# Kernel optimization log

Hardware: AMD Instinct MI355X
Metric: run time of the kernel (lower is better)

The kernel has to match this reference:

```python
import jax, jax.numpy as jnp
import numpy as np

B = 64      # num graphs
NPG = 800   # nodes per graph
N = B * NPG
EPG = 6400  # edges per graph (avg degree 8)
APG = 64    # feasible actions per graph
H = 4       # attention heads
C = 64      # hidden channels per head
OUT = 128   # out_channels


def _gat_params(key, fin, h, c, concat):
    k1, k2, k3 = jax.random.split(key, 3)
    s = 1.0 / np.sqrt(fin)
    W = jax.random.uniform(k1, (fin, h * c), jnp.float32, -s, s)
    a_src = jax.random.uniform(k2, (h, c), jnp.float32, -s, s)
    a_dst = jax.random.uniform(k3, (h, c), jnp.float32, -s, s)
    b = jnp.zeros((h * c if concat else c,), jnp.float32)
    return W, a_src, a_dst, b


def _lin_params(key, fin, fout):
    k1, k2 = jax.random.split(key)
    s = 1.0 / np.sqrt(fin)
    W = jax.random.uniform(k1, (fin, fout), jnp.float32, -s, s)
    b = jax.random.uniform(k2, (fout,), jnp.float32, -s, s)
    return W, b


def setup_inputs() -> dict:
    key = jax.random.key(0)
    ks = list(jax.random.split(key, 24))
    x = jax.random.normal(ks[0], (N, 5), jnp.float32)
    offs = jnp.arange(B, dtype=jnp.int32) * NPG
    src = jax.random.randint(ks[1], (B, EPG), 0, NPG, jnp.int32) + offs[:, None]
    dst = jax.random.randint(ks[2], (B, EPG), 0, NPG, jnp.int32) + offs[:, None]
    edge_index = jnp.stack([src.reshape(-1), dst.reshape(-1)])
    batch = jnp.repeat(jnp.arange(B, dtype=jnp.int32), NPG)
    actions_idx = (jax.random.randint(ks[3], (B, APG, 2), 0, NPG, jnp.int32)
                   + offs[:, None, None]).reshape(-1, 2)
    tabu_label = (jax.random.uniform(ks[4], (B * APG, 1)) < 0.5).astype(jnp.float32)
    inp = dict(x=x, edge_index=edge_index, batch=batch,
               actions_idx=actions_idx, tabu_label=tabu_label)
    names = ['f1', 'f2', 'f3', 'b1', 'b2', 'b3']
    fins = [3, H * C, H * C, 3, H * C, H * C]
    hs = [H, H, 1, H, H, 1]
    cs = [C, C, OUT, C, C, OUT]
    concats = [True, True, False, True, True, False]
    for i, nm in enumerate(names):
        W, a_s, a_d, b = _gat_params(ks[5 + i], fins[i], hs[i], cs[i], concats[i])
        inp[nm + '_W'] = W; inp[nm + '_as'] = a_s; inp[nm + '_ad'] = a_d; inp[nm + '_b'] = b
    dims = [(8 * OUT + 1, 2 * OUT), (2 * OUT, 2 * OUT), (2 * OUT, 2 * OUT), (2 * OUT, 1)]
    for i, (fi, fo) in enumerate(dims):
        W, b = _lin_params(ks[12 + i], fi, fo)
        inp['p_W%d' % (i + 1)] = W; inp['p_b%d' % (i + 1)] = b
    return inp


def _gat(h, s, d, W, a_src, a_dst, bias, concat):
    # PyG GATConv: project, per-edge attention, softmax over target index, scatter-add
    n = h.shape[0]
    Hh, Cc = a_src.shape
    xp = (h @ W).reshape(n, Hh, Cc)                      # [N,H,C]
    al_s = (xp * a_src).sum(-1)                          # [N,H]
    al_d = (xp * a_dst).sum(-1)                          # [N,H]
    e = jax.nn.leaky_relu(al_s[s] + al_d[d], 0.2)        # [E,H]
    m = jax.ops.segment_max(e, d, num_segments=n)
    ex = jnp.exp(e - m[d])
    den = jax.ops.segment_sum(ex, d, num_segments=n)
    alpha = ex / (den[d] + 1e-16)
    out = jax.ops.segment_sum(xp[s] * alpha[..., None], d, num_segments=n)  # [N,H,C]
    out = out.reshape(n, Hh * Cc) if concat else out.mean(axis=1)
    return out + bias


def reference(x, edge_index, batch, actions_idx, tabu_label,
              f1_W, f1_as, f1_ad, f1_b, f2_W, f2_as, f2_ad, f2_b,
              f3_W, f3_as, f3_ad, f3_b, b1_W, b1_as, b1_ad, b1_b,
              b2_W, b2_as, b2_ad, b2_b, b3_W, b3_as, b3_ad, b3_b,
              p_W1, p_b1, p_W2, p_b2, p_W3, p_b3, p_W4, p_b4):
    n = x.shape[0]
    ar = jnp.arange(n, dtype=edge_index.dtype)
    ei = jnp.concatenate([edge_index, jnp.stack([ar, ar])], axis=1)  # add_self_loops
    src, dst = ei[0], ei[1]
    # forward branch (flow source_to_target)
    hf = x[:, jnp.array([0, 1, 3])]
    hf = jax.nn.elu(_gat(hf, src, dst, f1_W, f1_as, f1_ad, f1_b, True))
    hf = jax.nn.elu(_gat(hf, src, dst, f2_W, f2_as, f2_ad, f2_b, True))
    hf3 = _gat(hf, src, dst, f3_W, f3_as, f3_ad, f3_b, False)
    # backward branch (flow target_to_source == reversed edges)
    hb = x[:, jnp.array([0, 2, 4])]
    hb = jax.nn.elu(_gat(hb, dst, src, b1_W, b1_as, b1_ad, b1_b, True))
    hb = jax.nn.elu(_gat(hb, dst, src, b2_W, b2_as, b2_ad, b2_b, True))
    hb3 = _gat(hb, dst, src, b3_W, b3_as, b3_ad, b3_b, False)
    h_node = jnp.concatenate([hf3, hb3], axis=-1)        # [N, 2*OUT]
    counts = jax.ops.segment_sum(jnp.ones((n,), x.dtype), batch, num_segments=B)
    g_pool = jax.ops.segment_sum(h_node, batch, num_segments=B) / counts[:, None]
    node_h = jnp.concatenate([h_node, g_pool[batch]], axis=-1)  # [N, 4*OUT]
    action_h = jnp.concatenate([node_h[actions_idx[:, 0]],
                                node_h[actions_idx[:, 1]],
                                tabu_label], axis=-1)    # [A, 8*OUT+1]
    h = jnp.tanh(action_h @ p_W1 + p_b1)
    h = jnp.tanh(h @ p_W2 + p_b2)
    h = jnp.tanh(h @ p_W3 + p_b3)
    score = (h @ p_W4 + p_b4).reshape(B, APG)
    log_prob = jax.nn.log_softmax(score, axis=-1)        # [B, APG]
    entropy = -(jnp.exp(log_prob) * log_prob).sum(-1, keepdims=True)  # [B,1]
    return (log_prob, entropy)
```

## Files before the change

kernel.cpp:

```cpp
#include <hip/hip_runtime.h>
#include <hip/hip_bf16.h>
#include <math.h>

constexpr int NN  = 51200;
constexpr int EE  = 409600;
constexpr int BB  = 64;
constexpr int APG = 64;
constexpr int NPG = 800;
constexpr int SCAN_N = 2 * NN;
constexpr int NA = BB * APG;
constexpr int KF = 1056;

typedef __bf16 bf16x8 __attribute__((ext_vector_type(8)));
typedef float f32x4 __attribute__((ext_vector_type(4)));
typedef float f32x2 __attribute__((ext_vector_type(2)));
typedef __attribute__((address_space(1))) const void g_void;
typedef __attribute__((address_space(3))) void l_void;

__device__ __forceinline__ float leaky(float x) { return x > 0.f ? x : 0.2f * x; }
__device__ __forceinline__ float bflo(unsigned w) { return __uint_as_float(w << 16); }
__device__ __forceinline__ float bfhi(unsigned w) { return __uint_as_float(w & 0xffff0000u); }
__device__ __forceinline__ unsigned short f2b(float x) {
  __hip_bfloat16 h = __float2bfloat16(x);
  unsigned short u;
  __builtin_memcpy(&u, &h, 2);
  return u;
}

__global__ void count_kernel(const int* __restrict__ ei, int* cnt) {
  int e = blockIdx.x * blockDim.x + threadIdx.x;
  if (e >= EE) return;
  int s = ei[e], d = ei[EE + e];
  atomicAdd(&cnt[d], 1);
  atomicAdd(&cnt[NN + s], 1);
}

__global__ __launch_bounds__(256) void scan1_kernel(const int* __restrict__ cnt,
                                                    int* __restrict__ rp,
                                                    int* __restrict__ bsum) {
  __shared__ int wsum[4];
  int b = blockIdx.x, t = threadIdx.x;
  int base = b * 1024 + t * 4;
  int4 v = *(const int4*)(cnt + base);
  int s = v.x + v.y + v.z + v.w;
  int lane = t & 63, wv = t >> 6;
  int incl = s;
  for (int off = 1; off < 64; off <<= 1) {
    int u = __shfl_up(incl, off);
    if (lane >= off) incl += u;
  }
  if (lane == 63) wsum[wv] = incl;
  __syncthreads();
  int woff = 0;
  for (int i = 0; i < wv; i++) woff += wsum[i];
  int excl = woff + incl - s;
  rp[base] = excl;
  rp[base + 1] = excl + v.x;
  rp[base + 2] = excl + v.x + v.y;
  rp[base + 3] = excl + v.x + v.y + v.z;
  if (t == 255) bsum[b] = woff + incl;
}

__global__ void scan2_kernel(const int* __restrict__ bsum, int* __restrict__ boff,
                             int* __restrict__ rp) {
  __shared__ int w0;
  int t = threadIdx.x;
  int v = (t < 100) ? bsum[t] : 0;
  int lane = t & 63;
  int incl = v;
  for (int off = 1; off < 64; off <<= 1) {
    int u = __shfl_up(incl, off);
    if (lane >= off) incl += u;
  }
  if (t == 63) w0 = incl;
  __syncthreads();
  int excl = incl - v + ((t >= 64) ? w0 : 0);
  if (t < 100) boff[t] = excl;
  if (t == 99) rp[SCAN_N] = excl + v;
}

__global__ __launch_bounds__(256) void scan3_kernel(int* __restrict__ rp,
                                                    const int* __restrict__ boff) {
  int b = blockIdx.x;
  int off = boff[b];
  int i = b * 1024 + threadIdx.x * 4;
  int4 v = *(int4*)(rp + i);
  v.x += off; v.y += off; v.z += off; v.w += off;
  *(int4*)(rp + i) = v;
}

__global__ void fill_kernel(const int* __restrict__ ei, const int* __restrict__ rp,
                            int* pos, int* __restrict__ col) {
  int e = blockIdx.x * blockDim.x + threadIdx.x;
  if (e >= EE) return;
  int s = ei[e], d = ei[EE + e];
  int p = atomicAdd(&pos[d], 1);
  col[rp[d] + p] = s;
  int q = atomicAdd(&pos[NN + s], 1);
  col[rp[NN + s] + q] = d;
}

__global__ __launch_bounds__(256) void lin1_al_kernel(const float* __restrict__ x,
                                                      const float* __restrict__ Wf,
                                                      const float* __restrict__ Wb,
                                                      const float* __restrict__ asf,
                                                      const float* __restrict__ asb,
                                                      const float* __restrict__ adf,
                                                      const float* __restrict__ adb,
                                                      __hip_bfloat16* __restrict__ out,
                                                      float* __restrict__ al_s,
                                                      float* __restrict__ al_d) {
  int n = blockIdx.x;
  bool bwd = n >= NN;
  int node = bwd ? n - NN : n;
  const float* W = bwd ? Wb : Wf;
  const float* a_src = bwd ? asb : asf;
  const float* a_dst = bwd ? adb : adf;
  int c1 = bwd ? 2 : 1, c2 = bwd ? 4 : 3;
  int j = threadIdx.x;
  int wv = j >> 6, lane = j & 63;
  float f0 = x[node * 5], f1 = x[node * 5 + c1], f2 = x[node * 5 + c2];
  float v = f0 * W[j] + f1 * W[256 + j] + f2 * W[512 + j];
  out[(size_t)n * 256 + j] = __float2bfloat16(v);
  float ps = v * a_src[j], pd = v * a_dst[j];
  for (int off = 1; off < 64; off <<= 1) {
    ps += __shfl_xor(ps, off);
    pd += __shfl_xor(pd, off);
  }
  if (lane == 0) {
    al_s[n * 4 + wv] = ps;
    al_d[n * 4 + wv] = pd;
  }
}

template <int HH>
__global__ __launch_bounds__(256) void alpha_kernel(const float* __restrict__ als,
                                                    const float* __restrict__ ald,
                                                    const int* __restrict__ rp,
                                                    const int* __restrict__ col,
                                                    float* __restrict__ alpha,
                                                    float* __restrict__ alpha_self) {
  int b = blockIdx.x;
  int xcd = b & 7, q = b >> 3;
  int g2 = (q / 25) * 8 + xcd;
  int d = g2 * 800 + (q % 25) * 32 + (threadIdx.x >> 3);
  int slot = threadIdx.x & 7;
  int off_row = (d >= NN) ? NN : 0;
  float ald_loc[HH], self_lg[HH];
#pragma unroll
  for (int h = 0; h < HH; h++) {
    ald_loc[h] = ald[d * HH + h];
    self_lg[h] = leaky(als[d * HH + h] + ald_loc[h]);
  }
  int beg = rp[d], end = rp[d + 1];
  int i0 = beg + slot;
  bool have = i0 < end;
  int s0 = col[have ? i0 : beg] + off_row;
  float mx[HH], lg0[HH];
#pragma unroll
  for (int h = 0; h < HH; h++) mx[h] = self_lg[h];
  if (have) {
#pragma unroll
    for (int h = 0; h < HH; h++) {
      lg0[h] = leaky(als[s0 * HH + h] + ald_loc[h]);
      mx[h] = fmaxf(mx[h], lg0[h]);
    }
  }
  for (int i = i0 + 8; i < end; i += 8) {
    int s = col[i] + off_row;
#pragma unroll
    for (int h = 0; h < HH; h++) mx[h] = fmaxf(mx[h], leaky(als[s * HH + h] + ald_loc[h]));
  }
#pragma unroll
  for (int h = 0; h < HH; h++) {
    mx[h] = fmaxf(mx[h], __shfl_xor(mx[h], 1));
    mx[h] = fmaxf(mx[h], __shfl_xor(mx[h], 2));
    mx[h] = fmaxf(mx[h], __shfl_xor(mx[h], 4));
  }
  float sm[HH], w0[HH];
#pragma unroll
  for (int h = 0; h < HH; h++) sm[h] = 0.f;
  if (have) {
#pragma unroll
    for (int h = 0; h < HH; h++) {
      w0[h] = __expf(lg0[h] - mx[h]);
      sm[h] += w0[h];
    }
  }
  for (int i = i0 + 8; i < end; i += 8) {
    int s = col[i] + off_row;
#pragma unroll
    for (int h = 0; h < HH; h++) {
      float w = __expf(leaky(als[s * HH + h] + ald_loc[h]) - mx[h]);
      sm[h] += w;
      alpha[(size_t)i * HH + h] = w;
    }
  }
#pragma unroll
  for (int h = 0; h < HH; h++) {
    sm[h] += __shfl_xor(sm[h], 1);
    sm[h] += __shfl_xor(sm[h], 2);
    sm[h] += __shfl_xor(sm[h], 4);
  }
  float inv[HH];
#pragma unroll
  for (int h = 0; h < HH; h++)
    inv[h] = 1.f / (sm[h] + __expf(self_lg[h] - mx[h]) + 1e-16f);
  if (have) {
#pragma unroll
    for (int h = 0; h < HH; h++) alpha[(size_t)i0 * HH + h] = w0[h] * inv[h];
  }
  for (int i = i0 + 8; i < end; i += 8)
#pragma unroll
    for (int h = 0; h < HH; h++) alpha[(size_t)i * HH + h] *= inv[h];
  if (slot == 0) {
#pragma unroll
    for (int h = 0; h < HH; h++)
      alpha_self[d * HH + h] = __expf(self_lg[h] - mx[h]) * inv[h];
  }
}

template <int ND>
__device__ __forceinline__ void load_dw(const unsigned* p, unsigned* w) {
  if constexpr (ND == 4) {
    uint4 v = *(const uint4*)p;
    w[0] = v.x; w[1] = v.y; w[2] = v.z; w[3] = v.w;
  } else {
    uint2 v = *(const uint2*)p;
    w[0] = v.x; w[1] = v.y;
  }
}
__device__ __forceinline__ f32x2 unpk(unsigned w) {
  f32x2 v;
  v.x = bflo(w);
  v.y = bfhi(w);
  return v;
}

template <int HH, int CC, int OUT_SPLIT>
__global__ __launch_bounds__(256) void spmm_kernel(const __hip_bfloat16* __restrict__ xp,
                                                   const float* __restrict__ alpha,
                                                   const float* __restrict__ alpha_self,
                                                   const int* __restrict__ rp,
                                                   const int* __restrict__ col,
                                                   const float* __restrict__ biasf,
                                                   const float* __restrict__ biasb,
                                                   __hip_bfloat16* __restrict__ out_bf,
                                                   int do_elu) {
  constexpr int HC = HH * CC;
  constexpr int CPL = HC / 32;
  constexpr int NW = CPL / 2;
  int b = blockIdx.x;
  int xcd = b & 7, q = b >> 3;
  int g2 = (q / 200) * 8 + xcd;
  int d = g2 * 800 + (q % 200) * 4 + (threadIdx.x >> 6);
  int off_row = (d >= NN) ? NN : 0;
  const float* bias = (d >= NN) ? biasb : biasf;
  int lane = threadIdx.x & 63;
  int sub = lane & 31, g = lane >> 5;
  int h_l = (sub * CPL) / CC;
  const unsigned* xw = (const unsigned*)xp;
  size_t rowoff = (size_t)sub * NW;
  f32x2 acc[NW];
#pragma unroll
  for (int j = 0; j < NW; j++) acc[j] = (f32x2)(0.f);
  int beg = rp[d], end = rp[d + 1];
  int deg = end - beg;
  if (g == 0) {
    float a = alpha_self[d * HH + h_l];
    unsigned w[NW];
    load_dw<NW>(xw + (size_t)d * (HC / 2) + rowoff, w);
#pragma unroll
    for (int q2 = 0; q2 < NW; q2++) acc[q2] += a * unpk(w[q2]);
  }
  for (int it = 0; it * 4 < deg; it++) {
    int e1 = beg + it * 4 + g;
    int e2 = e1 + 2;
    bool p1 = e1 < end, p2 = e2 < end;
    int ec1 = p1 ? e1 : beg, ec2 = p2 ? e2 : beg;
    int s1 = col[ec1] + off_row, s2 = col[ec2] + off_row;
    float a1 = p1 ? alpha[(size_t)ec1 * HH + h_l] : 0.f;
    float a2 = p2 ? alpha[(size_t)ec2 * HH + h_l] : 0.f;
    unsigned w1[NW], w2[NW];
    load_dw<NW>(xw + (size_t)s1 * (HC / 2) + rowoff, w1);
    load_dw<NW>(xw + (size_t)s2 * (HC / 2) + rowoff, w2);
#pragma unroll
    for (int q2 = 0; q2 < NW; q2++)
      acc[q2] += a1 * unpk(w1[q2]) + a2 * unpk(w2[q2]);
  }
#pragma unroll
  for (int j = 0; j < NW; j++) {
    acc[j].x += __shfl_xor(acc[j].x, 32);
    acc[j].y += __shfl_xor(acc[j].y, 32);
  }
  if (g == 0) {
    float v[CPL];
#pragma unroll
    for (int j = 0; j < NW; j++) {
      v[2 * j] = acc[j].x + bias[sub * CPL + 2 * j];
      v[2 * j + 1] = acc[j].y + bias[sub * CPL + 2 * j + 1];
    }
    if (do_elu) {
#pragma unroll
      for (int j = 0; j < CPL; j++) v[j] = v[j] > 0.f ? v[j] : (__expf(v[j]) - 1.f);
    }
    unsigned* ob;
    if constexpr (OUT_SPLIT) {
      int nd = (d < NN) ? d : d - NN;
      int oo = (d < NN) ? 0 : 64;
      ob = (unsigned*)out_bf + (size_t)nd * 128 + oo + sub * NW;
    } else {
      ob = (unsigned*)out_bf + (size_t)d * (HC / 2) + rowoff;
    }
#pragma unroll
    for (int q2 = 0; q2 < NW; q2++)
      ob[q2] = (unsigned)f2b(v[2 * q2]) | ((unsigned)f2b(v[2 * q2 + 1]) << 16);
  }
}

__global__ void castW2_kernel(const float* __restrict__ W0, const float* __restrict__ W1,
                              __hip_bfloat16* __restrict__ Wt0,
                              __hip_bfloat16* __restrict__ Wt1,
                              int K, int N, int Kp) {
  int idx = blockIdx.x * 256 + threadIdx.x;
  int tot = N * Kp;
  if (idx >= 2 * tot) return;
  const float* W = (idx < tot) ? W0 : W1;
  __hip_bfloat16* Wt = (idx < tot) ? Wt0 : Wt1;
  int i = (idx < tot) ? idx : idx - tot;
  int n = i / Kp, k = i % Kp;
  Wt[i] = (k < K) ? __float2bfloat16(W[(size_t)k * N + n]) : __float2bfloat16(0.f);
}

template <int EPI, int ALH, int ALCC>
__global__ __launch_bounds__(256) void gemm_mfma(const __hip_bfloat16* __restrict__ A,
                                                 const __hip_bfloat16* __restrict__ Bt0,
                                                 const __hip_bfloat16* __restrict__ Bt1,
                                                 __hip_bfloat16* __restrict__ Cb,
                                                 const float* __restrict__ bias0,
                                                 const float* __restrict__ bias1,
                                                 const float* __restrict__ asv0,
                                                 const float* __restrict__ asv1,
                                                 const float* __restrict__ adv0,
                                                 const float* __restrict__ adv1,
                                                 float* __restrict__ al_s,
                                                 float* __restrict__ al_d,
                                                 int M, int N, int K, int Mhalf) {
  __shared__ __align__(16) __hip_bfloat16 As[128 * 32];
  __shared__ __align__(16) __hip_bfloat16 Bs[128 * 32];
  int t = threadIdx.x;
  int wave = t >> 6, lane = t & 63;
  int wm = (wave >> 1) * 64, wn = (wave & 1) * 64;
  int bm = blockIdx.y * 128, bn = blockIdx.x * 128;
  bool second = bm >= Mhalf;
  const __hip_bfloat16* Bt = second ? Bt1 : Bt0;
  const float* bias = second ? bias1 : bias0;
  const float* asv = second ? asv1 : asv0;
  const float* adv = second ? adv1 : adv0;

  int r0 = t >> 2, c0 = (t & 3) * 8;
  const __hip_bfloat16* Ag0 = A + (size_t)(bm + r0) * K + c0;
  const __hip_bfloat16* Ag1 = A + (size_t)(bm + r0 + 64) * K + c0;
  const __hip_bfloat16* Bg0 = Bt + (size_t)(bn + r0) * K + c0;
  const __hip_bfloat16* Bg1 = Bt + (size_t)(bn + r0 + 64) * K + c0;
  __hip_bfloat16* Asp0 = As + t * 8;
  __hip_bfloat16* Asp1 = As + 64 * 8 * 4 + t * 8;
  __hip_bfloat16* Bsp0 = Bs + t * 8;
  __hip_bfloat16* Bsp1 = Bs + 64 * 8 * 4 + t * 8;

  f32x4 acc[4][4];
#pragma unroll
  for (int i = 0; i < 4; i++)
#pragma unroll
    for (int j = 0; j < 4; j++) acc[i][j] = (f32x4)(0.f);

  int frag_off = (lane & 15) * 32 + (lane >> 4) * 8;
  const __hip_bfloat16* Ab = As + wm * 32 + frag_off;
  const __hip_bfloat16* Bb = Bs + wn * 32 + frag_off;

  for (int k0 = 0; k0 < K; k0 += 32) {
    __syncthreads();
    __builtin_amdgcn_global_load_lds((g_void*)(Ag0 + k0), (l_void*)Asp0, 16, 0, 0);
    __builtin_amdgcn_global_load_lds((g_void*)(Ag1 + k0), (l_void*)Asp1, 16, 0, 0);
    __builtin_amdgcn_global_load_lds((g_void*)(Bg0 + k0), (l_void*)Bsp0, 16, 0, 0);
    __builtin_amdgcn_global_load_lds((g_void*)(Bg1 + k0), (l_void*)Bsp1, 16, 0, 0);
    __syncthreads();
    bf16x8 af[4], bfr[4];
#pragma unroll
    for (int i = 0; i < 4; i++) af[i] = *(const bf16x8*)(Ab + i * 16 * 32);
#pragma unroll
    for (int j = 0; j < 4; j++) bfr[j] = *(const bf16x8*)(Bb + j * 16 * 32);
#pragma unroll
    for (int i = 0; i < 4; i++)
#pragma unroll
      for (int j = 0; j < 4; j++)
        acc[i][j] = __builtin_amdgcn_mfma_f32_16x16x32_bf16(af[i], bfr[j], acc[i][j], 0, 0, 0);
  }

  int cr = (lane >> 4) * 4, cc = lane & 15;

  if constexpr (ALH > 0) {
    int head = (bn + wn) / ALCC;
    float as_c[4], ad_c[4];
#pragma unroll
    for (int j = 0; j < 4; j++) {
      int colx = bn + wn + j * 16 + cc;
      as_c[j] = asv[colx];
      ad_c[j] = adv[colx];
    }
#pragma unroll
    for (int i = 0; i < 4; i++)
#pragma unroll
      for (int r = 0; r < 4; r++) {
        float ps = 0.f, pd = 0.f;
#pragma unroll
        for (int j = 0; j < 4; j++) {
          ps += acc[i][j][r] * as_c[j];
          pd += acc[i][j][r] * ad_c[j];
        }
        ps += __shfl_xor(ps, 1); pd += __shfl_xor(pd, 1);
        ps += __shfl_xor(ps, 2); pd += __shfl_xor(pd, 2);
        ps += __shfl_xor(ps, 4); pd += __shfl_xor(pd, 4);
        ps += __shfl_xor(ps, 8); pd += __shfl_xor(pd, 8);
        if ((lane & 15) == 0) {
          int row = bm + wm + i * 16 + cr + r;
          if (ALCC > 64) {
            atomicAdd(&al_s[row * ALH + head], ps);
            atomicAdd(&al_d[row * ALH + head], pd);
          } else {
            al_s[row * ALH + head] = ps;
            al_d[row * ALH + head] = pd;
          }
        }
      }
  }

#pragma unroll
  for (int i = 0; i < 4; i++)
#pragma unroll
    for (int j = 0; j < 4; j++) {
      int colx = bn + wn + j * 16 + cc;
      float bs = (EPI == 2) ? bias[colx] : 0.f;
#pragma unroll
      for (int r = 0; r < 4; r++) {
        float v = acc[i][j][r];
        if (EPI == 2) v = tanhf(v + bs);
        Cb[(size_t)(bm + wm + i * 16 + cr + r) * N + colx] = __float2bfloat16(v);
      }
    }
}

__global__ void pool1_kernel(const __hip_bfloat16* __restrict__ h_node,
                             float* __restrict__ part) {
  int g = blockIdx.y, c = blockIdx.x, t = threadIdx.x;
  const unsigned* base = (const unsigned*)h_node + ((size_t)g * NPG + c * 100) * 128 + t;
  f32x2 s = (f32x2)(0.f);
  for (int i = 0; i < 100; i++) {
    unsigned w = base[(size_t)i * 128];
    s += unpk(w);
  }
  part[(size_t)(g * 8 + c) * 256 + 2 * t] = s.x;
  part[(size_t)(g * 8 + c) * 256 + 2 * t + 1] = s.y;
}

__global__ void pool2_kernel(const float* __restrict__ part, float* __restrict__ g_pool) {
  int g = blockIdx.x, t = threadIdx.x;
  float s = 0.f;
  for (int c = 0; c < 8; c++) s += part[(size_t)(g * 8 + c) * 256 + t];
  g_pool[g * 256 + t] = s * (1.f / NPG);
}

__global__ __launch_bounds__(256) void buildfeat_kernel(const __hip_bfloat16* __restrict__ h_node,
                                                        const float* __restrict__ g_pool,
                                                        const int* __restrict__ actions,
                                                        const float* __restrict__ tabu,
                                                        const int* __restrict__ batch,
                                                        __hip_bfloat16* __restrict__ feat) {
  int a = (blockIdx.x * blockDim.x + threadIdx.x) >> 6;
  int lane = threadIdx.x & 63;
  if (a >= NA) return;
  int n0 = actions[a * 2], n1 = actions[a * 2 + 1];
  int g = batch[n0];
  ushort4 v0 = *(const ushort4*)(h_node + (size_t)n0 * 256 + lane * 4);
  float4 vg = *(const float4*)(g_pool + (size_t)g * 256 + lane * 4);
  ushort4 v1 = *(const ushort4*)(h_node + (size_t)n1 * 256 + lane * 4);
  __hip_bfloat16* fr = feat + (size_t)a * KF;
  ushort4 ug = make_ushort4(f2b(vg.x), f2b(vg.y), f2b(vg.z), f2b(vg.w));
  *(ushort4*)(fr + lane * 4) = v0;
  *(ushort4*)(fr + 256 + lane * 4) = ug;
  *(ushort4*)(fr + 512 + lane * 4) = v1;
  *(ushort4*)(fr + 768 + lane * 4) = ug;
  if (lane < 8) {
    float t0 = (lane == 0) ? tabu[a] : 0.f;
    ushort4 u = make_ushort4(f2b(t0), 0, 0, 0);
    *(ushort4*)(fr + 1024 + lane * 4) = u;
  }
}

__global__ __launch_bounds__(256) void gemv_kernel(const __hip_bfloat16* __restrict__ y,
                                                   const float* __restrict__ W4,
                                                   const float* __restrict__ b4,
                                                   float* __restrict__ scores) {
  int a = (blockIdx.x * blockDim.x + threadIdx.x) >> 6;
  int lane = threadIdx.x & 63;
  if (a >= NA) return;
  const unsigned* row = (const unsigned*)(y + (size_t)a * 256);
  float s = 0.f;
#pragma unroll
  for (int q = 0; q < 2; q++) {
    unsigned w = row[lane * 2 + q];
    s += bflo(w) * W4[lane * 4 + 2 * q] + bfhi(w) * W4[lane * 4 + 2 * q + 1];
  }
  for (int off = 1; off < 64; off <<= 1) s += __shfl_xor(s, off);
  if (lane == 0) scores[a] = s + b4[0];
}

__global__ void softmax_kernel(const float* __restrict__ scores, float* __restrict__ out) {
  int g = (blockIdx.x * blockDim.x + threadIdx.x) >> 6;
  int lane = threadIdx.x & 63;
  if (g >= BB) return;
  float s = scores[g * 64 + lane];
  float m = s;
  for (int off = 1; off < 64; off <<= 1) m = fmaxf(m, __shfl_xor(m, off));
  float ex = expf(s - m);
  float sum = ex;
  for (int off = 1; off < 64; off <<= 1) sum += __shfl_xor(sum, off);
  float lp = s - m - logf(sum);
  out[g * 64 + lane] = lp;
  float pe = (ex / sum) * lp;
  for (int off = 1; off < 64; off <<= 1) pe += __shfl_xor(pe, off);
  if (lane == 0) out[BB * APG + g] = -pe;
}

extern "C" void kernel_launch(void* const* d_in, const int* in_sizes, int n_in,
                              void* d_out, int out_size, void* d_ws, size_t ws_size,
                              hipStream_t stream) {
  const float* x = (const float*)d_in[0];
  const int* ei = (const int*)d_in[1];
  const int* batch = (const int*)d_in[2];
  const int* actions = (const int*)d_in[3];
  const float* tabu = (const float*)d_in[4];
  const float* fW[3] = {(const float*)d_in[5], (const float*)d_in[9], (const float*)d_in[13]};
  const float* fas[3] = {(const float*)d_in[6], (const float*)d_in[10], (const float*)d_in[14]};
  const float* fad[3] = {(const float*)d_in[7], (const float*)d_in[11], (const float*)d_in[15]};
  const float* fb[3] = {(const float*)d_in[8], (const float*)d_in[12], (const float*)d_in[16]};
  const float* bW[3] = {(const float*)d_in[17], (const float*)d_in[21], (const float*)d_in[25]};
  const float* bas[3] = {(const float*)d_in[18], (const float*)d_in[22], (const float*)d_in[26]};
  const float* bad[3] = {(const float*)d_in[19], (const float*)d_in[23], (const float*)d_in[27]};
  const float* bb[3] = {(const float*)d_in[20], (const float*)d_in[24], (const float*)d_in[28]};
  const float* pW1 = (const float*)d_in[29];
  const float* pb1 = (const float*)d_in[30];
  const float* pW2 = (const float*)d_in[31];
  const float* pb2 = (const float*)d_in[32];
  const float* pW3 = (const float*)d_in[33];
  const float* pb3 = (const float*)d_in[34];
  const float* pW4 = (const float*)d_in[35];
  const float* pb4 = (const float*)d_in[36];
  float* out = (float*)d_out;

  char* ws = (char*)d_ws;
  size_t o = 0;
  auto alloc = [&](size_t bytes) -> void* {
    o = (o + 255) & ~(size_t)255;
    void* p = ws + o;
    o += bytes;
    return p;
  };
  int* cnt = (int*)alloc((size_t)4 * NN * 4);
  int* rp = (int*)alloc((size_t)(SCAN_N + 1) * 4);
  int* col = (int*)alloc(((size_t)2 * EE + 64) * 4);
  int* bsum = (int*)alloc(128 * 4);
  int* boff = (int*)alloc(128 * 4);
  float* al_s = (float*)alloc((size_t)SCAN_N * 4 * 4);
  float* al_d = (float*)alloc((size_t)SCAN_N * 4 * 4);
  float* alpha = (float*)alloc((size_t)2 * EE * 4 * 4);
  float* alpha_self = (float*)alloc((size_t)SCAN_N * 4 * 4);
  __hip_bfloat16* xp = (__hip_bfloat16*)alloc((size_t)SCAN_N * 256 * 2);
  __hip_bfloat16* bufA = (__hip_bfloat16*)alloc((size_t)SCAN_N * 256 * 2);
  __hip_bfloat16* h_node = (__hip_bfloat16*)alloc((size_t)NN * 256 * 2);
  __hip_bfloat16* wt0 = (__hip_bfloat16*)alloc((size_t)256 * KF * 2);
  __hip_bfloat16* wt1 = (__hip_bfloat16*)alloc((size_t)256 * KF * 2);
  float* part = (float*)alloc((size_t)BB * 8 * 256 * 4);
  float* g_pool = (float*)alloc((size_t)BB * 256 * 4);
  float* scores = (float*)alloc((size_t)NA * 4);
  __hip_bfloat16* feat = xp;
  __hip_bfloat16* y1 = feat + (size_t)NA * KF;
  __hip_bfloat16* y2 = y1 + (size_t)NA * 256;

  hipMemsetAsync(cnt, 0, (size_t)4 * NN * 4, stream);
  count_kernel<<<(EE + 255) / 256, 256, 0, stream>>>(ei, cnt);
  scan1_kernel<<<SCAN_N / 1024, 256, 0, stream>>>(cnt, rp, bsum);
  scan2_kernel<<<1, 128, 0, stream>>>(bsum, boff, rp);
  scan3_kernel<<<SCAN_N / 1024, 256, 0, stream>>>(rp, boff);
  fill_kernel<<<(EE + 255) / 256, 256, 0, stream>>>(ei, rp, cnt + 2 * NN, col);

  const int nwb = SCAN_N / 4;
  const int nab = SCAN_N * 8 / 256;

  lin1_al_kernel<<<SCAN_N, 256, 0, stream>>>(x, fW[0], bW[0], fas[0], bas[0],
                                             fad[0], bad[0], xp, al_s, al_d);
  alpha_kernel<4><<<nab, 256, 0, stream>>>(al_s, al_d, rp, col, alpha, alpha_self);
  spmm_kernel<4, 64, 0><<<nwb, 256, 0, stream>>>(xp, alpha, alpha_self, rp, col,
                                                 fb[0], bb[0], bufA, 1);
  castW2_kernel<<<(2 * 256 * 256 + 255) / 256, 256, 0, stream>>>(fW[1], bW[1], wt0, wt1,
                                                                 256, 256, 256);
  gemm_mfma<1, 4, 64><<<dim3(2, SCAN_N / 128), 256, 0, stream>>>(
      bufA, wt0, wt1, xp, nullptr, nullptr, fas[1], bas[1], fad[1], bad[1],
      al_s, al_d, SCAN_N, 256, 256, NN);
  alpha_kernel<4><<<nab, 256, 0, stream>>>(al_s, al_d, rp, col, alpha, alpha_self);
  spmm_kernel<4, 64, 0><<<nwb, 256, 0, stream>>>(xp, alpha, alpha_self, rp, col,
                                                 fb[1], bb[1], bufA, 1);
  castW2_kernel<<<(2 * 128 * 256 + 255) / 256, 256, 0, stream>>>(fW[2], bW[2], wt0, wt1,
                                                                 256, 128, 256);
  hipMemsetAsync(al_s, 0, (size_t)SCAN_N * 4, stream);
  hipMemsetAsync(al_d, 0, (size_t)SCAN_N * 4, stream);
  gemm_mfma<1, 1, 128><<<dim3(1, SCAN_N / 128), 256, 0, stream>>>(
      bufA, wt0, wt1, xp, nullptr, nullptr, fas[2], bas[2], fad[2], bad[2],
      al_s, al_d, SCAN_N, 128, 256, NN);
  alpha_kernel<1><<<nab, 256, 0, stream>>>(al_s, al_d, rp, col, alpha, alpha_self);
  spmm_kernel<1, 128, 1><<<nwb, 256, 0, stream>>>(xp, alpha, alpha_self, rp, col,
                                                  fb[2], bb[2], h_node, 0);

  pool1_kernel<<<dim3(8, BB), 128, 0, stream>>>(h_node, part);
  pool2_kernel<<<BB, 256, 0, stream>>>(part, g_pool);

  buildfeat_kernel<<<NA / 4, 256, 0, stream>>>(h_node, g_pool, actions, tabu, batch, feat);
  castW2_kernel<<<(256 * KF + 255) / 256, 256, 0, stream>>>(pW1, pW1, wt1, wt1, 1025, 256, KF / 2);
  castW2_kernel<<<(2 * 256 * KF + 255) / 256, 256, 0, stream>>>(pW1, pW1, wt0, wt1,
                                                                1025, 256, KF);
  gemm_mfma<2, 0, 64><<<dim3(2, NA / 128), 256, 0, stream>>>(
      feat, wt0, wt0, y1, pb1, pb1, nullptr, nullptr, nullptr, nullptr,
      nullptr, nullptr, NA, 256, KF, 1 << 30);
  castW2_kernel<<<(2 * 256 * 256 + 255) / 256, 256, 0, stream>>>(pW2, pW3, wt0, wt1,
                                                                 256, 256, 256);
  gemm_mfma<2, 0, 64><<<dim3(2, NA / 128), 256, 0, stream>>>(
      y1, wt0, wt0, y2, pb2, pb2, nullptr, nullptr, nullptr, nullptr,
      nullptr, nullptr, NA, 256, 256, 1 << 30);
  gemm_mfma<2, 0, 64><<<dim3(2, NA / 128), 256, 0, stream>>>(
      y2, wt1, wt1, y1, pb3, pb3, nullptr, nullptr, nullptr, nullptr,
      nullptr, nullptr, NA, 256, 256, 1 << 30);
  gemv_kernel<<<NA / 4, 256, 0, stream>>>(y1, pW4, pb4, scores);
  softmax_kernel<<<(BB * 64) / 256, 256, 0, stream>>>(scores, out);
}
```

Before: 574.3 us.

## Split first GAT layer: precompute W·a projections, vectorize lin1, drop redundant cast

The per-node attention logits of the first layer are computed algebraically from a tiny precomputed W·a table (3 inputs per head), so they no longer need a 64-lane reduction per head. The 256-wide linear transform runs in a separate kernel that writes 8 bf16 values per thread as 16-byte stores instead of one element per thread with one block per node. A redundant castW2 launch that another cast immediately overwrote is removed. The trade is two extra small launches. Computing the logits from fp32 inputs rather than the bf16-rounded features also changes rounding slightly.

```diff
diff --git a/kernel.cpp b/kernel.cpp
--- a/kernel.cpp
+++ b/kernel.cpp
@@ -25,6 +25,9 @@
   unsigned short u;
   __builtin_memcpy(&u, &h, 2);
   return u;
+}
+__device__ __forceinline__ unsigned pack2(float a, float b) {
+  return (unsigned)f2b(a) | ((unsigned)f2b(b) << 16);
 }
 
 __global__ void count_kernel(const int* __restrict__ ei, int* cnt) {
@@ -100,37 +103,62 @@
   col[rp[NN + s] + q] = d;
 }
 
-__global__ __launch_bounds__(256) void lin1_al_kernel(const float* __restrict__ x,
-                                                      const float* __restrict__ Wf,
+__global__ __launch_bounds__(256) void precomp_kernel(const float* __restrict__ Wf,
                                                       const float* __restrict__ Wb,
                                                       const float* __restrict__ asf,
+                                                      const float* __restrict__ adf,
                                                       const float* __restrict__ asb,
-                                                      const float* __restrict__ adf,
                                                       const float* __restrict__ adb,
-                                                      __hip_bfloat16* __restrict__ out,
-                                                      float* __restrict__ al_s,
-                                                      float* __restrict__ al_d) {
-  int n = blockIdx.x;
-  bool bwd = n >= NN;
-  int node = bwd ? n - NN : n;
-  const float* W = bwd ? Wb : Wf;
-  const float* a_src = bwd ? asb : asf;
-  const float* a_dst = bwd ? adb : adf;
-  int c1 = bwd ? 2 : 1, c2 = bwd ? 4 : 3;
-  int j = threadIdx.x;
-  int wv = j >> 6, lane = j & 63;
+                                                      float* __restrict__ wa) {
+  int wave = (blockIdx.x * blockDim.x + threadIdx.x) >> 6;
+  int lane = threadIdx.x & 63;
+  if (wave >= 48) return;
+  int dir = wave / 24, sd = (wave / 12) % 2, h = (wave / 3) % 4, c = wave % 3;
+  const float* W = dir ? Wb : Wf;
+  const float* a = dir ? (sd ? adb : asb) : (sd ? adf : asf);
+  float v = W[c * 256 + h * 64 + lane] * a[h * 64 + lane];
+  for (int off = 1; off < 64; off <<= 1) v += __shfl_xor(v, off);
+  if (lane == 0) wa[wave] = v;
+}
+
+__global__ __launch_bounds__(256) void lin1_kernel(const float* __restrict__ x,
+                                                   const float* __restrict__ Wf,
+                                                   const float* __restrict__ Wb,
+                                                   __hip_bfloat16* __restrict__ out) {
+  int idx = blockIdx.x * 256 + threadIdx.x;
+  int n = idx >> 5, grp = idx & 31;
+  int dir = (n >= NN) ? 1 : 0;
+  int node = dir ? n - NN : n;
+  const float* W = dir ? Wb : Wf;
+  int c1 = dir ? 2 : 1, c2 = dir ? 4 : 3;
   float f0 = x[node * 5], f1 = x[node * 5 + c1], f2 = x[node * 5 + c2];
-  float v = f0 * W[j] + f1 * W[256 + j] + f2 * W[512 + j];
-  out[(size_t)n * 256 + j] = __float2bfloat16(v);
-  float ps = v * a_src[j], pd = v * a_dst[j];
-  for (int off = 1; off < 64; off <<= 1) {
-    ps += __shfl_xor(ps, off);
-    pd += __shfl_xor(pd, off);
-  }
-  if (lane == 0) {
-    al_s[n * 4 + wv] = ps;
-    al_d[n * 4 + wv] = pd;
-  }
+  int j0 = grp * 8;
+  float v[8];
+#pragma unroll
+  for (int j = 0; j < 8; j++)
+    v[j] = f0 * W[j0 + j] + f1 * W[256 + j0 + j] + f2 * W[512 + j0 + j];
+  uint4 u;
+  u.x = pack2(v[0], v[1]);
+  u.y = pack2(v[2], v[3]);
+  u.z = pack2(v[4], v[5]);
+  u.w = pack2(v[6], v[7]);
+  *(uint4*)(out + (size_t)n * 256 + j0) = u;
+}
+
+__global__ __launch_bounds__(256) void al1_kernel(const float* __restrict__ x,
+                                                  const float* __restrict__ wa,
+                                                  float* __restrict__ al_s,
+                                                  float* __restrict__ al_d) {
+  int idx = blockIdx.x * 256 + threadIdx.x;
+  int n = idx >> 2, h = idx & 3;
+  int dir = (n >= NN) ? 1 : 0;
+  int node = dir ? n - NN : n;
+  int c1 = dir ? 2 : 1, c2 = dir ? 4 : 3;
+  float f0 = x[node * 5], f1 = x[node * 5 + c1], f2 = x[node * 5 + c2];
+  const float* ws = wa + dir * 24 + h * 3;
+  const float* wd = wa + dir * 24 + 12 + h * 3;
+  al_s[idx] = f0 * ws[0] + f1 * ws[1] + f2 * ws[2];
+  al_d[idx] = f0 * wd[0] + f1 * wd[1] + f2 * wd[2];
 }
 
 template <int HH>
@@ -314,7 +342,7 @@
     }
 #pragma unroll
     for (int q2 = 0; q2 < NW; q2++)
-      ob[q2] = (unsigned)f2b(v[2 * q2]) | ((unsigned)f2b(v[2 * q2 + 1]) << 16);
+      ob[q2] = pack2(v[2 * q2], v[2 * q2 + 1]);
   }
 }
 
@@ -575,6 +603,7 @@
   float* al_d = (float*)alloc((size_t)SCAN_N * 4 * 4);
   float* alpha = (float*)alloc((size_t)2 * EE * 4 * 4);
   float* alpha_self = (float*)alloc((size_t)SCAN_N * 4 * 4);
+  float* wa = (float*)alloc(64 * 4);
   __hip_bfloat16* xp = (__hip_bfloat16*)alloc((size_t)SCAN_N * 256 * 2);
   __hip_bfloat16* bufA = (__hip_bfloat16*)alloc((size_t)SCAN_N * 256 * 2);
   __hip_bfloat16* h_node = (__hip_bfloat16*)alloc((size_t)NN * 256 * 2);
@@ -597,8 +626,9 @@
   const int nwb = SCAN_N / 4;
   const int nab = SCAN_N * 8 / 256;
 
-  lin1_al_kernel<<<SCAN_N, 256, 0, stream>>>(x, fW[0], bW[0], fas[0], bas[0],
-                                             fad[0], bad[0], xp, al_s, al_d);
+  precomp_kernel<<<12, 256, 0, stream>>>(fW[0], bW[0], fas[0], fad[0], bas[0], bad[0], wa);
+  lin1_kernel<<<SCAN_N * 32 / 256, 256, 0, stream>>>(x, fW[0], bW[0], xp);
+  al1_kernel<<<SCAN_N * 4 / 256, 256, 0, stream>>>(x, wa, al_s, al_d);
   alpha_kernel<4><<<nab, 256, 0, stream>>>(al_s, al_d, rp, col, alpha, alpha_self);
   spmm_kernel<4, 64, 0><<<nwb, 256, 0, stream>>>(xp, alpha, alpha_self, rp, col,
                                                  fb[0], bb[0], bufA, 1);
@@ -625,7 +655,6 @@
   pool2_kernel<<<BB, 256, 0, stream>>>(part, g_pool);
 
   buildfeat_kernel<<<NA / 4, 256, 0, stream>>>(h_node, g_pool, actions, tabu, batch, feat);
-  castW2_kernel<<<(256 * KF + 255) / 256, 256, 0, stream>>>(pW1, pW1, wt1, wt1, 1025, 256, KF / 2);
   castW2_kernel<<<(2 * 256 * KF + 255) / 256, 256, 0, stream>>>(pW1, pW1, wt0, wt1,
                                                                 1025, 256, KF);
   gemm_mfma<2, 0, 64><<<dim3(2, NA / 128), 256, 0, stream>>>(
```

Result: faster. 536.4 us (-6.6%).
